# Kernel tuning notes

Hardware: AMD Instinct MI355X
Metric: run time of the kernel (lower is better)

Reference implementation:

```python
import jax, jax.numpy as jnp
import numpy as np
from jax import lax

B, N, S, K = 16, 4096, 1024, 32
C_PTS = 64
MLP = [64, 64, 128]
BN_EPS = 1e-5


def _fps(xyz, npoint):
    """Farthest point sampling. xyz: [B,N,3] -> idx [B,npoint] int32."""
    b, n, _ = xyz.shape
    def body(carry, _):
        dist, farthest = carry                       # [B,N], [B]
        centroid = xyz[jnp.arange(b), farthest]      # [B,3]
        d = jnp.sum((xyz - centroid[:, None, :]) ** 2, axis=-1)  # [B,N]
        dist = jnp.minimum(dist, d)
        nxt = jnp.argmax(dist, axis=-1).astype(jnp.int32)
        return (dist, nxt), farthest
    init = (jnp.full((b, n), 1e10, dtype=xyz.dtype), jnp.zeros((b,), jnp.int32))
    _, idxs = lax.scan(body, init, None, length=npoint)  # [npoint, B]
    return idxs.T


def _gather(pts, idx):
    """pts: [B,N,C], idx: [B,S,K] -> [B,S,K,C] (per-batch gather)."""
    return jax.vmap(lambda p, i: p[i])(pts, idx)


def setup_inputs() -> dict:
    key = jax.random.key(0)
    ks = jax.random.split(key, 16)
    inp = {
        "xyz": jax.random.normal(ks[0], (B, N, 3), jnp.float32),
        "points": jax.random.normal(ks[1], (B, N, C_PTS), jnp.float32),
    }
    last = 3 + C_PTS
    ki = 2
    for i, out_c in enumerate(MLP):
        scale = 1.0 / np.sqrt(last)
        inp[f"w{i}"] = jax.random.normal(ks[ki], (last, out_c), jnp.float32) * scale
        inp[f"b{i}"] = jnp.zeros((out_c,), jnp.float32)
        inp[f"g{i}"] = jnp.ones((out_c,), jnp.float32)
        inp[f"be{i}"] = jnp.zeros((out_c,), jnp.float32)
        last = out_c
        ki += 1
    return inp


def _forward(xyz, points, params):
    fps_idx = _fps(xyz, S)                                    # [B,S]
    new_xyz = jnp.take_along_axis(xyz, fps_idx[..., None], axis=1)  # [B,S,3]
    # KNN: pairwise squared distances centroids -> all points
    d = (jnp.sum(new_xyz ** 2, -1)[:, :, None]
         - 2.0 * jnp.einsum('bsc,bnc->bsn', new_xyz, xyz)
         + jnp.sum(xyz ** 2, -1)[:, None, :])                 # [B,S,N]
    _, knn_idx = lax.top_k(-d, K)                             # [B,S,K]
    grouped_xyz = _gather(xyz, knn_idx) - new_xyz[:, :, None, :]   # [B,S,K,3]
    grouped_pts = _gather(points, knn_idx)                    # [B,S,K,C]
    x = jnp.concatenate([grouped_xyz, grouped_pts], axis=-1)  # [B,S,K,3+C]
    for (w, b, g, be) in params:
        x = jnp.einsum('bskc,cd->bskd', x, w) + b             # 1x1 conv
        mean = jnp.mean(x, axis=(0, 1, 2))                    # BN (train stats)
        var = jnp.var(x, axis=(0, 1, 2))
        x = (x - mean) * lax.rsqrt(var + BN_EPS) * g + be
        x = jax.nn.relu(x)
    new_points = jnp.max(x, axis=2)                           # max over nsample
    return new_xyz, new_points


def reference(xyz, points, w0, b0, g0, be0, w1, b1, g1, be1, w2, b2, g2, be2):
    params = [(w0, b0, g0, be0), (w1, b1, g1, be1), (w2, b2, g2, be2)]
    return _forward(xyz, points, params)
```

## Files before the change

### kernel.cpp

```cpp
#include <hip/hip_runtime.h>
#include <float.h>
#include <math.h>

#define B_ 16
#define N_ 4096
#define S_ 1024
#define K_ 32
#define CIN0 67
#define NBS (B_ * S_)
#define NEWXYZ_FLOATS (B_ * S_ * 3)
#define AST 68


__device__ __forceinline__ float sqdist3(float x, float y, float z,
                                         float cx, float cy, float cz) {
#pragma clang fp contract(off)
  float dx = x - cx, dy = y - cy, dz = z - cz;
  float s = dx * dx;
  s = s + dy * dy;
  s = s + dz * dz;
  return s;
}

__device__ __forceinline__ float knn_dist(float c2, float cx, float cy, float cz,
                                          float x, float y, float z) {
#pragma clang fp contract(off)
  float dot = cx * x; dot = dot + cy * y; dot = dot + cz * z;
  float x2 = x * x;   x2 = x2 + y * y;   x2 = x2 + z * z;
  float d = c2 - 2.0f * dot;
  d = d + x2;
  return d;
}

template <int CTRL>
__device__ __forceinline__ float dpp_f(float v, float oldv) {
  return __int_as_float(__builtin_amdgcn_update_dpp(
      __float_as_int(oldv), __float_as_int(v), CTRL, 0xF, 0xF, false));
}
template <int CTRL>
__device__ __forceinline__ int dpp_i(int v, int oldv) {
  return __builtin_amdgcn_update_dpp(oldv, v, CTRL, 0xF, 0xF, false);
}

template <int CTRL>
__device__ __forceinline__ void fps_combine2(float& val, int& idx) {
  const float tv = dpp_f<CTRL>(val, -1.0f);
  const int ti = dpp_i<CTRL>(idx, 0x7fffffff);
  const bool take = (tv > val) || (tv == val && ti < idx);
  val = take ? tv : val;
  idx = take ? ti : idx;
}

__global__ __launch_bounds__(256, 1) void fps_kernel(
    const float* __restrict__ xyz, float* __restrict__ newxyz) {
  const int b = blockIdx.x;
  const int t = threadIdx.x;
  __shared__ float4 sp[N_];
  __shared__ float2 rec[2][4];
  __shared__ float cbuf[S_ * 3];
  const float* xb = xyz + (size_t)b * N_ * 3;
  for (int p = t; p < N_; p += 256) {
    sp[p] = make_float4(xb[p * 3 + 0], xb[p * 3 + 1], xb[p * 3 + 2], 0.0f);
  }
  float ax[16], ay[16], az[16];
#pragma unroll
  for (int j = 0; j < 16; ++j) {
    const int p = t * 16 + j;
    const float x = xb[p * 3 + 0];
    const float y = xb[p * 3 + 1];
    const float z = xb[p * 3 + 2];
    asm volatile("v_accvgpr_write_b32 %0, %1" : "=a"(ax[j]) : "v"(x));
    asm volatile("v_accvgpr_write_b32 %0, %1" : "=a"(ay[j]) : "v"(y));
    asm volatile("v_accvgpr_write_b32 %0, %1" : "=a"(az[j]) : "v"(z));
  }
  float dist[16];
#pragma unroll
  for (int j = 0; j < 16; ++j) dist[j] = 1e10f;
  __syncthreads();
  float cx = xb[0], cy = xb[1], cz = xb[2];
  for (int s = 0; s < S_; ++s) {
    if (t == 0) {
      cbuf[s * 3 + 0] = cx;
      cbuf[s * 3 + 1] = cy;
      cbuf[s * 3 + 2] = cz;
    }
    float dd[16];
#pragma unroll
    for (int j = 0; j < 16; ++j) {
      float x, y, z;
      asm volatile("v_accvgpr_read_b32 %0, %1" : "=v"(x) : "a"(ax[j]));
      asm volatile("v_accvgpr_read_b32 %0, %1" : "=v"(y) : "a"(ay[j]));
      asm volatile("v_accvgpr_read_b32 %0, %1" : "=v"(z) : "a"(az[j]));
      dd[j] = sqdist3(x, y, z, cx, cy, cz);
    }
    __builtin_amdgcn_sched_barrier(0);
    float best = -1.0f;
    int bi = 0;
#pragma unroll
    for (int j = 0; j < 16; ++j) {
      const float nd = fminf(dist[j], dd[j]);
      dist[j] = nd;
      const bool take = nd > best;
      best = take ? nd : best;
      bi = take ? (t * 16 + j) : bi;
    }
    fps_combine2<0x111>(best, bi);
    fps_combine2<0x112>(best, bi);
    fps_combine2<0x114>(best, bi);
    fps_combine2<0x118>(best, bi);
    fps_combine2<0x142>(best, bi);
    fps_combine2<0x143>(best, bi);
    const float wv = __int_as_float(__builtin_amdgcn_readlane(__float_as_int(best), 63));
    const int wi = __builtin_amdgcn_readlane(bi, 63);
    const int par = s & 1;
    if ((t & 63) == 0) {
      rec[par][t >> 6] = make_float2(wv, __int_as_float(wi));
    }
    __syncthreads();
    float2 r0 = rec[par][0];
    float bv = r0.x;
    int bj = __float_as_int(r0.y);
#pragma unroll
    for (int w = 1; w < 4; ++w) {
      const float2 r = rec[par][w];
      const int iw = __float_as_int(r.y);
      const bool take = (r.x > bv) || (r.x == bv && iw < bj);
      bv = take ? r.x : bv;
      bj = take ? iw : bj;
    }
    const float4 c = sp[bj];
    cx = c.x; cy = c.y; cz = c.z;
  }
  __syncthreads();
  float* ob = newxyz + (size_t)b * S_ * 3;
  for (int i = t; i < S_ * 3; i += 256) ob[i] = cbuf[i];
}

__global__ __launch_bounds__(256, 2) void knn_kernel(
    const float* __restrict__ xyz, const float* __restrict__ newxyz,
    int* __restrict__ knn_idx) {
  const int bs0 = blockIdx.x * 4;
  const int b = bs0 >> 10;
  const int t = threadIdx.x;
  const int wave = t >> 6;
  const int lane = t & 63;
  __shared__ float sxx[N_];
  __shared__ float sxy[N_];
  __shared__ float sxz[N_];
  const float* xb = xyz + (size_t)b * N_ * 3;
  for (int p = t; p < N_; p += 256) {
    sxx[p] = xb[p * 3 + 0];
    sxy[p] = xb[p * 3 + 1];
    sxz[p] = xb[p * 3 + 2];
  }
  __syncthreads();
  const int bs = bs0 + wave;
  const float cx = newxyz[(size_t)bs * 3 + 0];
  const float cy = newxyz[(size_t)bs * 3 + 1];
  const float cz = newxyz[(size_t)bs * 3 + 2];
  float c2;
  {
#pragma clang fp contract(off)
    float s = cx * cx;
    s = s + cy * cy;
    s = s + cz * cz;
    c2 = s;
  }
  float d[64];
  float gval[8];
  int gidx[8];
#pragma unroll
  for (int g = 0; g < 8; ++g) {
    float gv = FLT_MAX;
    int gi = g * 8;
#pragma unroll
    for (int q = 0; q < 8; ++q) {
      const int j = g * 8 + q;
      const int p = j * 64 + lane;
      const float dd = knn_dist(c2, cx, cy, cz, sxx[p], sxy[p], sxz[p]);
      d[j] = dd;
      if (dd < gv) { gv = dd; gi = j; }
    }
    gval[g] = gv; gidx[g] = gi;
  }
  int* krow = knn_idx + (size_t)bs * K_;
  for (int it = 0; it < K_; ++it) {
    float best = gval[0];
    int bj = gidx[0];
#pragma unroll
    for (int g = 1; g < 8; ++g) {
      if (gval[g] < best || (gval[g] == best && gidx[g] < bj)) { best = gval[g]; bj = gidx[g]; }
    }
    int bidx = bj * 64 + lane;
#pragma unroll
    for (int off = 32; off >= 1; off >>= 1) {
      const float ov = __shfl_xor(best, off);
      const int oi = __shfl_xor(bidx, off);
      if (ov < best || (ov == best && oi < bidx)) { best = ov; bidx = oi; }
    }
    if (lane == 0) krow[it] = bidx;
    if (lane == (bidx & 63)) {
      const int jl = bidx >> 6;
      const int gg = jl >> 3;
      const int qq = jl & 7;
#pragma unroll
      for (int g = 0; g < 8; ++g) {
        if (g == gg) {
#pragma unroll
          for (int q = 0; q < 8; ++q) {
            d[g * 8 + q] = (q == qq) ? FLT_MAX : d[g * 8 + q];
          }
          float gv = FLT_MAX;
          int gi = g * 8;
#pragma unroll
          for (int q = 0; q < 8; ++q) {
            const int j = g * 8 + q;
            if (d[j] < gv) { gv = d[j]; gi = j; }
          }
          gval[g] = gv; gidx[g] = gi;
        }
      }
    }
  }
}


__device__ __forceinline__ void loadw(float* __restrict__ wbuf,
                                      const float* __restrict__ w, int n, int t) {
  for (int i = t; i < n; i += 256) wbuf[i] = w[i];
}

__device__ __forceinline__ void loadw_half(float* __restrict__ wbuf,
                                           const float* __restrict__ w2, int ofs, int t) {
  for (int i = t; i < 64 * 64; i += 256) {
    const int c = i >> 6, j = i & 63;
    wbuf[i] = w2[c * 128 + ofs + j];
  }
}

__device__ __forceinline__ void build_x0(float* __restrict__ act,
    const float* __restrict__ xyz, const float* __restrict__ points,
    const int* __restrict__ knn_idx, const float* __restrict__ newxyz,
    int bs, int t) {
  const int b = bs >> 10;
  const int* krow = knn_idx + (size_t)bs * K_;
  const float cx = newxyz[(size_t)bs * 3 + 0];
  const float cy = newxyz[(size_t)bs * 3 + 1];
  const float cz = newxyz[(size_t)bs * 3 + 2];
  for (int i = t; i < K_ * CIN0; i += 256) {
    const int k = i / CIN0;
    const int c = i - k * CIN0;
    const int p = krow[k];
    float v;
    if (c < 3) {
      v = xyz[((size_t)b * N_ + p) * 3 + c] - (c == 0 ? cx : (c == 1 ? cy : cz));
    } else {
      v = points[((size_t)b * N_ + p) * 64 + (c - 3)];
    }
    act[k * AST + c] = v;
  }
}

template <int CIN>
__device__ __forceinline__ void matmul64(const float* __restrict__ act,
    const float* __restrict__ wbuf, const float* __restrict__ bias,
    float* __restrict__ out, int t) {
  const int k = t >> 3;
  const int g = t & 7;
  float acc[8];
#pragma unroll
  for (int j = 0; j < 8; ++j) acc[j] = bias[g * 8 + j];
  for (int c = 0; c < CIN; ++c) {
    const float xv = act[k * AST + c];
    const float4 wa = *(const float4*)&wbuf[c * 64 + g * 8];
    const float4 wb = *(const float4*)&wbuf[c * 64 + g * 8 + 4];
    acc[0] += xv * wa.x; acc[1] += xv * wa.y;
    acc[2] += xv * wa.z; acc[3] += xv * wa.w;
    acc[4] += xv * wb.x; acc[5] += xv * wb.y;
    acc[6] += xv * wb.z; acc[7] += xv * wb.w;
  }
  *(float4*)&out[k * AST + g * 8] = make_float4(acc[0], acc[1], acc[2], acc[3]);
  *(float4*)&out[k * AST + g * 8 + 4] = make_float4(acc[4], acc[5], acc[6], acc[7]);
}

__device__ __forceinline__ void norm_relu64(float* __restrict__ act,
    const float* __restrict__ scale, const float* __restrict__ shift, int t) {
  for (int i = t; i < K_ * 64; i += 256) {
    const int k = i >> 6, c = i & 63;
    const float v = act[k * AST + c] * scale[c] + shift[c];
    act[k * AST + c] = fmaxf(v, 0.0f);
  }
}

__device__ __forceinline__ void stats64(const float* __restrict__ out,
    float* __restrict__ psum, float* __restrict__ psq, int bs, int ofs, int t) {
  if (t < 64) {
    float s = 0.f, q = 0.f;
    for (int k = 0; k < K_; ++k) {
      const float v = out[k * AST + t];
      s += v; q += v * v;
    }
    psum[(size_t)bs * 128 + ofs + t] = s;
    psq[(size_t)bs * 128 + ofs + t] = q;
  }
}

__device__ __forceinline__ void minmax64(const float* __restrict__ out,
    float* __restrict__ maxraw, float* __restrict__ minbuf, int bs, int ofs, int t) {
  if (t >= 64 && t < 128) {
    const int ch = t - 64;
    float mx = -FLT_MAX, mn = FLT_MAX;
    for (int k = 0; k < K_; ++k) {
      const float v = out[k * AST + ch];
      mx = fmaxf(mx, v); mn = fminf(mn, v);
    }
    maxraw[(size_t)bs * 128 + ofs + ch] = mx;
    minbuf[(size_t)bs * 128 + ofs + ch] = mn;
  }
}


__global__ __launch_bounds__(256) void passA_store_kernel(
    const float* __restrict__ xyz, const float* __restrict__ points,
    const float* __restrict__ newxyz, const int* __restrict__ knn_idx,
    const float* __restrict__ w0, const float* __restrict__ b0,
    float* __restrict__ psum, float* __restrict__ psq, float* __restrict__ zbuf) {
  __shared__ __align__(16) float actA[K_ * AST];
  __shared__ __align__(16) float outB[K_ * AST];
  __shared__ __align__(16) float wbuf[CIN0 * 64];
  const int bs = blockIdx.x, t = threadIdx.x;
  build_x0(actA, xyz, points, knn_idx, newxyz, bs, t);
  loadw(wbuf, w0, CIN0 * 64, t);
  __syncthreads();
  matmul64<CIN0>(actA, wbuf, b0, outB, t);
  __syncthreads();
  stats64(outB, psum, psq, bs, 0, t);
  float* zrow = zbuf + (size_t)bs * 2048;
  for (int i = t; i < 2048; i += 256) zrow[i] = outB[(i >> 6) * AST + (i & 63)];
}

__global__ __launch_bounds__(256) void passB_z_kernel(
    const float* __restrict__ w1, const float* __restrict__ b1,
    const float* __restrict__ scales, const float* __restrict__ shifts,
    float* __restrict__ psum, float* __restrict__ psq, float* __restrict__ zbuf) {
  __shared__ __align__(16) float actA[K_ * AST];
  __shared__ __align__(16) float outB[K_ * AST];
  __shared__ __align__(16) float wbuf[64 * 64];
  const int bs = blockIdx.x, t = threadIdx.x;
  float* zrow = zbuf + (size_t)bs * 2048;
  for (int i = t; i < 2048; i += 256) outB[(i >> 6) * AST + (i & 63)] = zrow[i];
  loadw(wbuf, w1, 64 * 64, t);
  __syncthreads();
  norm_relu64(outB, scales, shifts, t);
  __syncthreads();
  matmul64<64>(outB, wbuf, b1, actA, t);
  __syncthreads();
  stats64(actA, psum, psq, bs, 0, t);
  for (int i = t; i < 2048; i += 256) zrow[i] = actA[(i >> 6) * AST + (i & 63)];
}

__global__ __launch_bounds__(256) void passC_z_kernel(
    const float* __restrict__ w2, const float* __restrict__ b2,
    const float* __restrict__ scales1, const float* __restrict__ shifts1,
    float* __restrict__ psum, float* __restrict__ psq,
    float* __restrict__ maxraw, float* __restrict__ minbuf,
    const float* __restrict__ zbuf) {
  __shared__ __align__(16) float actA[K_ * AST];
  __shared__ __align__(16) float outB[K_ * AST];
  __shared__ __align__(16) float wbuf[64 * 64];
  const int bs = blockIdx.x, t = threadIdx.x;
  const float* zrow = zbuf + (size_t)bs * 2048;
  for (int i = t; i < 2048; i += 256) actA[(i >> 6) * AST + (i & 63)] = zrow[i];
  loadw_half(wbuf, w2, 0, t);
  __syncthreads();
  norm_relu64(actA, scales1, shifts1, t);
  __syncthreads();
  matmul64<64>(actA, wbuf, b2, outB, t);
  __syncthreads();
  stats64(outB, psum, psq, bs, 0, t);
  minmax64(outB, maxraw, minbuf, bs, 0, t);
  loadw_half(wbuf, w2, 64, t);
  __syncthreads();
  matmul64<64>(actA, wbuf, b2 + 64, outB, t);
  __syncthreads();
  stats64(outB, psum, psq, bs, 64, t);
  minmax64(outB, maxraw, minbuf, bs, 64, t);
}


__global__ __launch_bounds__(256) void passA_kernel(
    const float* __restrict__ xyz, const float* __restrict__ points,
    const float* __restrict__ newxyz, const int* __restrict__ knn_idx,
    const float* __restrict__ w0, const float* __restrict__ b0,
    float* __restrict__ psum, float* __restrict__ psq) {
  __shared__ __align__(16) float actA[K_ * AST];
  __shared__ __align__(16) float outB[K_ * AST];
  __shared__ __align__(16) float wbuf[CIN0 * 64];
  const int bs = blockIdx.x, t = threadIdx.x;
  build_x0(actA, xyz, points, knn_idx, newxyz, bs, t);
  loadw(wbuf, w0, CIN0 * 64, t);
  __syncthreads();
  matmul64<CIN0>(actA, wbuf, b0, outB, t);
  __syncthreads();
  stats64(outB, psum, psq, bs, 0, t);
}

__global__ __launch_bounds__(256) void passB_kernel(
    const float* __restrict__ xyz, const float* __restrict__ points,
    const float* __restrict__ newxyz, const int* __restrict__ knn_idx,
    const float* __restrict__ w0, const float* __restrict__ b0,
    const float* __restrict__ w1, const float* __restrict__ b1,
    const float* __restrict__ scales, const float* __restrict__ shifts,
    float* __restrict__ psum, float* __restrict__ psq) {
  __shared__ __align__(16) float actA[K_ * AST];
  __shared__ __align__(16) float outB[K_ * AST];
  __shared__ __align__(16) float wbuf[CIN0 * 64];
  const int bs = blockIdx.x, t = threadIdx.x;
  build_x0(actA, xyz, points, knn_idx, newxyz, bs, t);
  loadw(wbuf, w0, CIN0 * 64, t);
  __syncthreads();
  matmul64<CIN0>(actA, wbuf, b0, outB, t);
  __syncthreads();
  norm_relu64(outB, scales, shifts, t);
  loadw(wbuf, w1, 64 * 64, t);
  __syncthreads();
  matmul64<64>(outB, wbuf, b1, actA, t);
  __syncthreads();
  stats64(actA, psum, psq, bs, 0, t);
}

__global__ __launch_bounds__(256) void passC_kernel(
    const float* __restrict__ xyz, const float* __restrict__ points,
    const float* __restrict__ newxyz, const int* __restrict__ knn_idx,
    const float* __restrict__ w0, const float* __restrict__ b0,
    const float* __restrict__ w1, const float* __restrict__ b1,
    const float* __restrict__ w2, const float* __restrict__ b2,
    const float* __restrict__ scales, const float* __restrict__ shifts,
    float* __restrict__ psum, float* __restrict__ psq,
    float* __restrict__ maxraw, float* __restrict__ minbuf) {
  __shared__ __align__(16) float actA[K_ * AST];
  __shared__ __align__(16) float outB[K_ * AST];
  __shared__ __align__(16) float wbuf[CIN0 * 64];
  const int bs = blockIdx.x, t = threadIdx.x;
  build_x0(actA, xyz, points, knn_idx, newxyz, bs, t);
  loadw(wbuf, w0, CIN0 * 64, t);
  __syncthreads();
  matmul64<CIN0>(actA, wbuf, b0, outB, t);
  __syncthreads();
  norm_relu64(outB, scales, shifts, t);
  loadw(wbuf, w1, 64 * 64, t);
  __syncthreads();
  matmul64<64>(outB, wbuf, b1, actA, t);
  __syncthreads();
  norm_relu64(actA, scales + 128, shifts + 128, t);
  loadw_half(wbuf, w2, 0, t);
  __syncthreads();
  matmul64<64>(actA, wbuf, b2, outB, t);
  __syncthreads();
  stats64(outB, psum, psq, bs, 0, t);
  minmax64(outB, maxraw, minbuf, bs, 0, t);
  loadw_half(wbuf, w2, 64, t);
  __syncthreads();
  matmul64<64>(actA, wbuf, b2 + 64, outB, t);
  __syncthreads();
  stats64(outB, psum, psq, bs, 64, t);
  minmax64(outB, maxraw, minbuf, bs, 64, t);
}

__global__ __launch_bounds__(256) void finalize_kernel(
    const float* __restrict__ psum, const float* __restrict__ psq,
    const float* __restrict__ g, const float* __restrict__ be,
    float* __restrict__ scale, float* __restrict__ shift) {
  const int ch = blockIdx.x, t = threadIdx.x;
  __shared__ float ss[256];
  __shared__ float sq[256];
  float s = 0.f, q = 0.f;
  for (int p = t; p < NBS; p += 256) {
    s += psum[(size_t)p * 128 + ch];
    q += psq[(size_t)p * 128 + ch];
  }
  ss[t] = s; sq[t] = q;
  __syncthreads();
  for (int off = 128; off >= 1; off >>= 1) {
    if (t < off) { ss[t] += ss[t + off]; sq[t] += sq[t + off]; }
    __syncthreads();
  }
  if (t == 0) {
    const float invN = 1.0f / (float)(B_ * S_ * K_);
    const float mean = ss[0] * invN;
    const float var = sq[0] * invN - mean * mean;
    const float sc = g[ch] / sqrtf(var + 1e-5f);
    scale[ch] = sc;
    shift[ch] = be[ch] - mean * sc;
  }
}

__global__ __launch_bounds__(256) void final_kernel(
    const float* __restrict__ minbuf, const float* __restrict__ scale,
    const float* __restrict__ shift, float* __restrict__ out) {
  const int i = blockIdx.x * 256 + threadIdx.x;
  const int ch = i & 127;
  const float sc = scale[ch], sh = shift[ch];
  const float mx = out[NEWXYZ_FLOATS + i];
  const float mn = minbuf[i];
  const float v = sc * (sc >= 0.f ? mx : mn) + sh;
  out[NEWXYZ_FLOATS + i] = fmaxf(v, 0.f);
}

extern "C" void kernel_launch(void* const* d_in, const int* in_sizes, int n_in,
                              void* d_out, int out_size, void* d_ws, size_t ws_size,
                              hipStream_t stream) {
  const float* xyz = (const float*)d_in[0];
  const float* points = (const float*)d_in[1];
  const float* w0 = (const float*)d_in[2];
  const float* b0 = (const float*)d_in[3];
  const float* g0 = (const float*)d_in[4];
  const float* be0 = (const float*)d_in[5];
  const float* w1 = (const float*)d_in[6];
  const float* b1 = (const float*)d_in[7];
  const float* g1 = (const float*)d_in[8];
  const float* be1 = (const float*)d_in[9];
  const float* w2 = (const float*)d_in[10];
  const float* b2 = (const float*)d_in[11];
  const float* g2 = (const float*)d_in[12];
  const float* be2 = (const float*)d_in[13];
  float* out = (float*)d_out;
  float* newxyz = out;
  float* maxraw = out + NEWXYZ_FLOATS;

  float* ws = (float*)d_ws;
  const size_t NEED_FAST =
      (size_t)(524288 + 16384 * 2048 + 2 * NBS * 128 + 768 + NBS * 128) * 4;

  fps_kernel<<<B_, 256, 0, stream>>>(xyz, newxyz);

  if (ws_size >= NEED_FAST) {
    int* knn_idx = (int*)ws;
    float* zbuf = ws + 524288;
    float* psum = zbuf + (size_t)16384 * 2048;
    float* psq = psum + (size_t)NBS * 128;
    float* scales = psq + (size_t)NBS * 128;
    float* shifts = scales + 384;
    float* minbuf = shifts + 384;
    knn_kernel<<<NBS / 4, 256, 0, stream>>>(xyz, newxyz, knn_idx);
    passA_store_kernel<<<NBS, 256, 0, stream>>>(xyz, points, newxyz, knn_idx, w0, b0,
                                                psum, psq, zbuf);
    finalize_kernel<<<64, 256, 0, stream>>>(psum, psq, g0, be0, scales, shifts);
    passB_z_kernel<<<NBS, 256, 0, stream>>>(w1, b1, scales, shifts, psum, psq, zbuf);
    finalize_kernel<<<64, 256, 0, stream>>>(psum, psq, g1, be1, scales + 128, shifts + 128);
    passC_z_kernel<<<NBS, 256, 0, stream>>>(w2, b2, scales + 128, shifts + 128,
                                            psum, psq, maxraw, minbuf, zbuf);
    finalize_kernel<<<128, 256, 0, stream>>>(psum, psq, g2, be2, scales + 256, shifts + 256);
    final_kernel<<<(B_ * S_ * 128) / 256, 256, 0, stream>>>(minbuf, scales + 256,
                                                            shifts + 256, out);
  } else {
    int* knn_idx = (int*)ws;
    float* psum = ws + 524288;
    float* psq = psum + (size_t)NBS * 128;
    float* scales = psq + (size_t)NBS * 128;
    float* shifts = scales + 384;
    float* minbuf = shifts + 384;
    knn_kernel<<<NBS / 4, 256, 0, stream>>>(xyz, newxyz, knn_idx);
    passA_kernel<<<NBS, 256, 0, stream>>>(xyz, points, newxyz, knn_idx, w0, b0, psum, psq);
    finalize_kernel<<<64, 256, 0, stream>>>(psum, psq, g0, be0, scales, shifts);
    passB_kernel<<<NBS, 256, 0, stream>>>(xyz, points, newxyz, knn_idx, w0, b0, w1, b1,
                                          scales, shifts, psum, psq);
    finalize_kernel<<<64, 256, 0, stream>>>(psum, psq, g1, be1, scales + 128, shifts + 128);
    passC_kernel<<<NBS, 256, 0, stream>>>(xyz, points, newxyz, knn_idx, w0, b0, w1, b1, w2, b2,
                                          scales, shifts, psum, psq, maxraw, minbuf);
    finalize_kernel<<<128, 256, 0, stream>>>(psum, psq, g2, be2, scales + 256, shifts + 256);
    final_kernel<<<(B_ * S_ * 128) / 256, 256, 0, stream>>>(minbuf, scales + 256,
                                                            shifts + 256, out);
  }
}
```

Before: 2.009 ms.

## Process four centroid groups per block with register-tiled MLP matmuls

The three MLP pass kernels now handle four (b,s) groups per block instead of one. Each wave owns one group and computes a 4x8 register tile per thread with float4 LDS reads, so the weight tile loaded into shared memory is reused four times. BN statistics and max/min are reduced with wave shuffles instead of shared-memory passes. Normalisation and ReLU are fused into the zbuf load, and the layer-0 weights are padded to 68 input channels so the vector loads stay aligned. The cost is higher register pressure and a larger shared-memory footprint per block, with launch bounds set to two blocks per CU.

```diff
diff --git a/kernel.cpp b/kernel.cpp
--- a/kernel.cpp
+++ b/kernel.cpp
@@ -10,6 +10,8 @@
 #define NBS (B_ * S_)
 #define NEWXYZ_FLOATS (B_ * S_ * 3)
 #define AST 68
+#define AQ (K_ * AST)
+#define QB 4
 
 
 __device__ __forceinline__ float sqdist3(float x, float y, float z,
@@ -225,17 +227,227 @@
 }
 
 
-__device__ __forceinline__ void loadw(float* __restrict__ wbuf,
-                                      const float* __restrict__ w, int n, int t) {
-  for (int i = t; i < n; i += 256) wbuf[i] = w[i];
-}
-
+__device__ __forceinline__ void loadw0p(float* __restrict__ wbuf,
+                                        const float* __restrict__ w0, int t) {
+  for (int i = t; i < 68 * 64; i += 256) {
+    const int c = i >> 6;
+    wbuf[i] = (c < 67) ? w0[i] : 0.0f;
+  }
+}
+__device__ __forceinline__ void loadw64(float* __restrict__ wbuf,
+                                        const float* __restrict__ w, int t) {
+  for (int i = t; i < 64 * 64; i += 256) wbuf[i] = w[i];
+}
 __device__ __forceinline__ void loadw_half(float* __restrict__ wbuf,
                                            const float* __restrict__ w2, int ofs, int t) {
   for (int i = t; i < 64 * 64; i += 256) {
     const int c = i >> 6, j = i & 63;
     wbuf[i] = w2[c * 128 + ofs + j];
   }
+}
+
+__device__ __forceinline__ void build4(float* __restrict__ act,
+    const float* __restrict__ xyz, const float* __restrict__ points,
+    const int* __restrict__ knn_idx, const float* __restrict__ newxyz,
+    int bs0, int t) {
+  const int b = bs0 >> 10;
+  for (int i = t; i < QB * K_ * AST; i += 256) {
+    const int q = i / AQ;
+    const int rem = i - q * AQ;
+    const int k = rem / AST;
+    const int c = rem - k * AST;
+    const int bs = bs0 + q;
+    const int p = knn_idx[(size_t)bs * K_ + k];
+    float v;
+    if (c < 3) {
+      v = xyz[((size_t)b * N_ + p) * 3 + c] - newxyz[(size_t)bs * 3 + c];
+    } else if (c < 67) {
+      v = points[((size_t)b * N_ + p) * 64 + (c - 3)];
+    } else {
+      v = 0.0f;
+    }
+    act[i] = v;
+  }
+}
+
+template <int CQ>
+__device__ __forceinline__ void mm4(const float* __restrict__ actq,
+    const float* __restrict__ wbuf, const float* __restrict__ bias,
+    float acc[4][8], int kslot, int g) {
+#pragma unroll
+  for (int j = 0; j < 8; ++j) {
+    const float bj = bias[g * 8 + j];
+#pragma unroll
+    for (int i = 0; i < 4; ++i) acc[i][j] = bj;
+  }
+  for (int qd = 0; qd < CQ; ++qd) {
+    float4 a[4];
+#pragma unroll
+    for (int i = 0; i < 4; ++i)
+      a[i] = *(const float4*)&actq[(kslot * 4 + i) * AST + qd * 4];
+#pragma unroll
+    for (int cc = 0; cc < 4; ++cc) {
+      const float4 wlo = *(const float4*)&wbuf[(qd * 4 + cc) * 64 + g * 8];
+      const float4 whi = *(const float4*)&wbuf[(qd * 4 + cc) * 64 + g * 8 + 4];
+#pragma unroll
+      for (int i = 0; i < 4; ++i) {
+        const float x = (cc == 0) ? a[i].x : (cc == 1) ? a[i].y
+                        : (cc == 2) ? a[i].z : a[i].w;
+        acc[i][0] += x * wlo.x;
+        acc[i][1] += x * wlo.y;
+        acc[i][2] += x * wlo.z;
+        acc[i][3] += x * wlo.w;
+        acc[i][4] += x * whi.x;
+        acc[i][5] += x * whi.y;
+        acc[i][6] += x * whi.z;
+        acc[i][7] += x * whi.w;
+      }
+    }
+  }
+}
+
+__device__ __forceinline__ void stats4(const float acc[4][8],
+    float* __restrict__ psum, float* __restrict__ psq, int bs, int ofs, int r) {
+  float s[8], ss[8];
+#pragma unroll
+  for (int j = 0; j < 8; ++j) {
+    s[j] = ((acc[0][j] + acc[1][j]) + acc[2][j]) + acc[3][j];
+    ss[j] = ((acc[0][j] * acc[0][j] + acc[1][j] * acc[1][j]) +
+             acc[2][j] * acc[2][j]) + acc[3][j] * acc[3][j];
+  }
+#pragma unroll
+  for (int m = 8; m <= 32; m <<= 1) {
+#pragma unroll
+    for (int j = 0; j < 8; ++j) {
+      s[j] += __shfl_xor(s[j], m);
+      ss[j] += __shfl_xor(ss[j], m);
+    }
+  }
+  if (r < 8) {
+#pragma unroll
+    for (int j = 0; j < 8; ++j) {
+      psum[(size_t)bs * 128 + ofs + r * 8 + j] = s[j];
+      psq[(size_t)bs * 128 + ofs + r * 8 + j] = ss[j];
+    }
+  }
+}
+
+__device__ __forceinline__ void minmax4(const float acc[4][8],
+    float* __restrict__ maxraw, float* __restrict__ minbuf, int bs, int ofs, int r) {
+  float mx[8], mn[8];
+#pragma unroll
+  for (int j = 0; j < 8; ++j) {
+    mx[j] = fmaxf(fmaxf(acc[0][j], acc[1][j]), fmaxf(acc[2][j], acc[3][j]));
+    mn[j] = fminf(fminf(acc[0][j], acc[1][j]), fminf(acc[2][j], acc[3][j]));
+  }
+#pragma unroll
+  for (int m = 8; m <= 32; m <<= 1) {
+#pragma unroll
+    for (int j = 0; j < 8; ++j) {
+      mx[j] = fmaxf(mx[j], __shfl_xor(mx[j], m));
+      mn[j] = fminf(mn[j], __shfl_xor(mn[j], m));
+    }
+  }
+  if (r < 8) {
+#pragma unroll
+    for (int j = 0; j < 8; ++j) {
+      maxraw[(size_t)bs * 128 + ofs + r * 8 + j] = mx[j];
+      minbuf[(size_t)bs * 128 + ofs + r * 8 + j] = mn[j];
+    }
+  }
+}
+
+__device__ __forceinline__ void zstore4(const float acc[4][8],
+    float* __restrict__ zrow, int kslot, int g) {
+#pragma unroll
+  for (int i = 0; i < 4; ++i) {
+    const int base = (kslot * 4 + i) * 64 + g * 8;
+    *(float4*)&zrow[base] = make_float4(acc[i][0], acc[i][1], acc[i][2], acc[i][3]);
+    *(float4*)&zrow[base + 4] = make_float4(acc[i][4], acc[i][5], acc[i][6], acc[i][7]);
+  }
+}
+
+
+__global__ __launch_bounds__(256, 2) void passA4_kernel(
+    const float* __restrict__ xyz, const float* __restrict__ points,
+    const float* __restrict__ newxyz, const int* __restrict__ knn_idx,
+    const float* __restrict__ w0, const float* __restrict__ b0,
+    float* __restrict__ psum, float* __restrict__ psq, float* __restrict__ zbuf) {
+  __shared__ __align__(16) float act[QB * AQ];
+  __shared__ __align__(16) float wbuf[68 * 64];
+  const int bs0 = blockIdx.x * QB, t = threadIdx.x;
+  build4(act, xyz, points, knn_idx, newxyz, bs0, t);
+  loadw0p(wbuf, w0, t);
+  __syncthreads();
+  const int q = t >> 6, r = t & 63, ks = r >> 3, g = r & 7;
+  float acc[4][8];
+  mm4<17>(act + q * AQ, wbuf, b0, acc, ks, g);
+  stats4(acc, psum, psq, bs0 + q, 0, r);
+  zstore4(acc, zbuf + (size_t)(bs0 + q) * 2048, ks, g);
+}
+
+__global__ __launch_bounds__(256, 2) void passB4_kernel(
+    const float* __restrict__ w1, const float* __restrict__ b1,
+    const float* __restrict__ scales, const float* __restrict__ shifts,
+    float* __restrict__ psum, float* __restrict__ psq, float* __restrict__ zbuf) {
+  __shared__ __align__(16) float act[QB * AQ];
+  __shared__ __align__(16) float wbuf[64 * 64];
+  const int bs0 = blockIdx.x * QB, t = threadIdx.x;
+  const float* zb = zbuf + (size_t)bs0 * 2048;
+  for (int i = t; i < QB * 2048; i += 256) {
+    const int q2 = i >> 11;
+    const int rem = i & 2047;
+    const int k = rem >> 6;
+    const int c = rem & 63;
+    const float v = zb[i] * scales[c] + shifts[c];
+    act[q2 * AQ + k * AST + c] = fmaxf(v, 0.0f);
+  }
+  loadw64(wbuf, w1, t);
+  __syncthreads();
+  const int q = t >> 6, r = t & 63, ks = r >> 3, g = r & 7;
+  float acc[4][8];
+  mm4<16>(act + q * AQ, wbuf, b1, acc, ks, g);
+  stats4(acc, psum, psq, bs0 + q, 0, r);
+  zstore4(acc, zbuf + (size_t)(bs0 + q) * 2048, ks, g);
+}
+
+__global__ __launch_bounds__(256, 2) void passC4_kernel(
+    const float* __restrict__ w2, const float* __restrict__ b2,
+    const float* __restrict__ scales1, const float* __restrict__ shifts1,
+    float* __restrict__ psum, float* __restrict__ psq,
+    float* __restrict__ maxraw, float* __restrict__ minbuf,
+    const float* __restrict__ zbuf) {
+  __shared__ __align__(16) float act[QB * AQ];
+  __shared__ __align__(16) float wbuf[64 * 64];
+  const int bs0 = blockIdx.x * QB, t = threadIdx.x;
+  const float* zb = zbuf + (size_t)bs0 * 2048;
+  for (int i = t; i < QB * 2048; i += 256) {
+    const int q2 = i >> 11;
+    const int rem = i & 2047;
+    const int k = rem >> 6;
+    const int c = rem & 63;
+    const float v = zb[i] * scales1[c] + shifts1[c];
+    act[q2 * AQ + k * AST + c] = fmaxf(v, 0.0f);
+  }
+  loadw_half(wbuf, w2, 0, t);
+  __syncthreads();
+  const int q = t >> 6, r = t & 63, ks = r >> 3, g = r & 7;
+  float acc[4][8];
+  mm4<16>(act + q * AQ, wbuf, b2, acc, ks, g);
+  stats4(acc, psum, psq, bs0 + q, 0, r);
+  minmax4(acc, maxraw, minbuf, bs0 + q, 0, r);
+  __syncthreads();
+  loadw_half(wbuf, w2, 64, t);
+  __syncthreads();
+  mm4<16>(act + q * AQ, wbuf, b2 + 64, acc, ks, g);
+  stats4(acc, psum, psq, bs0 + q, 64, r);
+  minmax4(acc, maxraw, minbuf, bs0 + q, 64, r);
+}
+
+
+__device__ __forceinline__ void loadw(float* __restrict__ wbuf,
+                                      const float* __restrict__ w, int n, int t) {
+  for (int i = t; i < n; i += 256) wbuf[i] = w[i];
 }
 
 __device__ __forceinline__ void build_x0(float* __restrict__ act,
@@ -318,75 +530,6 @@
     minbuf[(size_t)bs * 128 + ofs + ch] = mn;
   }
 }
-
-
-__global__ __launch_bounds__(256) void passA_store_kernel(
-    const float* __restrict__ xyz, const float* __restrict__ points,
-    const float* __restrict__ newxyz, const int* __restrict__ knn_idx,
-    const float* __restrict__ w0, const float* __restrict__ b0,
-    float* __restrict__ psum, float* __restrict__ psq, float* __restrict__ zbuf) {
-  __shared__ __align__(16) float actA[K_ * AST];
-  __shared__ __align__(16) float outB[K_ * AST];
-  __shared__ __align__(16) float wbuf[CIN0 * 64];
-  const int bs = blockIdx.x, t = threadIdx.x;
-  build_x0(actA, xyz, points, knn_idx, newxyz, bs, t);
-  loadw(wbuf, w0, CIN0 * 64, t);
-  __syncthreads();
-  matmul64<CIN0>(actA, wbuf, b0, outB, t);
-  __syncthreads();
-  stats64(outB, psum, psq, bs, 0, t);
-  float* zrow = zbuf + (size_t)bs * 2048;
-  for (int i = t; i < 2048; i += 256) zrow[i] = outB[(i >> 6) * AST + (i & 63)];
-}
-
-__global__ __launch_bounds__(256) void passB_z_kernel(
-    const float* __restrict__ w1, const float* __restrict__ b1,
-    const float* __restrict__ scales, const float* __restrict__ shifts,
-    float* __restrict__ psum, float* __restrict__ psq, float* __restrict__ zbuf) {
-  __shared__ __align__(16) float actA[K_ * AST];
-  __shared__ __align__(16) float outB[K_ * AST];
-  __shared__ __align__(16) float wbuf[64 * 64];
-  const int bs = blockIdx.x, t = threadIdx.x;
-  float* zrow = zbuf + (size_t)bs * 2048;
-  for (int i = t; i < 2048; i += 256) outB[(i >> 6) * AST + (i & 63)] = zrow[i];
-  loadw(wbuf, w1, 64 * 64, t);
-  __syncthreads();
-  norm_relu64(outB, scales, shifts, t);
-  __syncthreads();
-  matmul64<64>(outB, wbuf, b1, actA, t);
-  __syncthreads();
-  stats64(actA, psum, psq, bs, 0, t);
-  for (int i = t; i < 2048; i += 256) zrow[i] = actA[(i >> 6) * AST + (i & 63)];
-}
-
-__global__ __launch_bounds__(256) void passC_z_kernel(
-    const float* __restrict__ w2, const float* __restrict__ b2,
-    const float* __restrict__ scales1, const float* __restrict__ shifts1,
-    float* __restrict__ psum, float* __restrict__ psq,
-    float* __restrict__ maxraw, float* __restrict__ minbuf,
-    const float* __restrict__ zbuf) {
-  __shared__ __align__(16) float actA[K_ * AST];
-  __shared__ __align__(16) float outB[K_ * AST];
-  __shared__ __align__(16) float wbuf[64 * 64];
-  const int bs = blockIdx.x, t = threadIdx.x;
-  const float* zrow = zbuf + (size_t)bs * 2048;
-  for (int i = t; i < 2048; i += 256) actA[(i >> 6) * AST + (i & 63)] = zrow[i];
-  loadw_half(wbuf, w2, 0, t);
-  __syncthreads();
-  norm_relu64(actA, scales1, shifts1, t);
-  __syncthreads();
-  matmul64<64>(actA, wbuf, b2, outB, t);
-  __syncthreads();
-  stats64(outB, psum, psq, bs, 0, t);
-  minmax64(outB, maxraw, minbuf, bs, 0, t);
-  loadw_half(wbuf, w2, 64, t);
-  __syncthreads();
-  matmul64<64>(actA, wbuf, b2 + 64, outB, t);
-  __syncthreads();
-  stats64(outB, psum, psq, bs, 64, t);
-  minmax64(outB, maxraw, minbuf, bs, 64, t);
-}
-
 
 __global__ __launch_bounds__(256) void passA_kernel(
     const float* __restrict__ xyz, const float* __restrict__ points,
@@ -543,13 +686,13 @@
     float* shifts = scales + 384;
     float* minbuf = shifts + 384;
     knn_kernel<<<NBS / 4, 256, 0, stream>>>(xyz, newxyz, knn_idx);
-    passA_store_kernel<<<NBS, 256, 0, stream>>>(xyz, points, newxyz, knn_idx, w0, b0,
+    passA4_kernel<<<NBS / QB, 256, 0, stream>>>(xyz, points, newxyz, knn_idx, w0, b0,
                                                 psum, psq, zbuf);
     finalize_kernel<<<64, 256, 0, stream>>>(psum, psq, g0, be0, scales, shifts);
-    passB_z_kernel<<<NBS, 256, 0, stream>>>(w1, b1, scales, shifts, psum, psq, zbuf);
+    passB4_kernel<<<NBS / QB, 256, 0, stream>>>(w1, b1, scales, shifts, psum, psq, zbuf);
     finalize_kernel<<<64, 256, 0, stream>>>(psum, psq, g1, be1, scales + 128, shifts + 128);
-    passC_z_kernel<<<NBS, 256, 0, stream>>>(w2, b2, scales + 128, shifts + 128,
-                                            psum, psq, maxraw, minbuf, zbuf);
+    passC4_kernel<<<NBS / QB, 256, 0, stream>>>(w2, b2, scales + 128, shifts + 128,
+                                                psum, psq, maxraw, minbuf, zbuf);
     finalize_kernel<<<128, 256, 0, stream>>>(psum, psq, g2, be2, scales + 256, shifts + 256);
     final_kernel<<<(B_ * S_ * 128) / 256, 256, 0, stream>>>(minbuf, scales + 256,
                                                             shifts + 256, out);
```

Result: faster. 1.866 ms, median of 2 (-7.1%).
